# Kernel tuning notes

Measured on AMD Instinct MI355X. Metric: run time of the kernel, lower is better.

## Reference

```python
import jax, jax.numpy as jnp
import numpy as np

E = 131072      # edges per key
MUL = 64        # multiplicity in '64x0e+64x1o'
FEA = MUL * 4   # 64 scalars + 64*3 vector components = 256
RAD = 64        # edge-length embedding width (64x0e)
HID = 128       # MLP hidden (128x0e)
WNUM = 4 * MUL  # 4 uvu paths x 64 per-channel weights = 256


def _mlp(x, W1, b1, g, be, W2):
    # Linear -> LayerNorm -> Gate(silu on scalars) -> last Linear (no bias)
    h = x @ W1 + b1
    mu = h.mean(-1, keepdims=True)
    var = h.var(-1, keepdims=True)
    h = (h - mu) / jnp.sqrt(var + 1e-5) * g + be
    return jax.nn.silu(h) @ W2


def _dtp(fea, vec, w):
    # depthwise (uvu) tensor product of (64x0e+64x1o) x (1x0e+1x1o) -> (64x0e+64x1o)
    x0 = fea[:, :MUL]                       # [E, 64]   0e part
    x1 = fea[:, MUL:].reshape(-1, MUL, 3)   # [E, 64, 3] 1o part
    y0 = vec[:, 0]                          # [E]       0e
    y1 = vec[:, 1:4]                        # [E, 3]    1o
    w1, w2, w3, w4 = jnp.split(w, 4, axis=1)  # each [E, 64]
    inv_s3 = 1.0 / jnp.sqrt(jnp.asarray(3.0, fea.dtype))  # CG(1,1,0) = delta/sqrt(3)
    inv_s2 = 1.0 / jnp.sqrt(jnp.asarray(2.0, fea.dtype))  # per-output path normalization (2 paths each)
    out0 = (w1 * x0 * y0[:, None]
            + w4 * jnp.einsum('eud,ed->eu', x1, y1) * inv_s3) * inv_s2
    out1 = (w2[:, :, None] * x0[:, :, None] * y1[:, None, :]
            + w3[:, :, None] * x1 * y0[:, None, None]) * inv_s2
    return jnp.concatenate([out0, out1.reshape(-1, MUL * 3)], axis=1)


def setup_inputs() -> dict:
    key = jax.random.key(0)
    ks = jax.random.split(key, 16)
    d = {}
    for i, k in enumerate(['a', 'b']):
        d[f'edge_fea_{k}'] = jax.random.normal(ks[i * 3 + 0], (E, FEA), jnp.float32)
        d[f'edge_vec_{k}'] = jax.random.normal(ks[i * 3 + 1], (E, 4), jnp.float32)
        d[f'edge_len_{k}'] = jax.random.uniform(ks[i * 3 + 2], (E, RAD), jnp.float32)
        d[f'W1_{k}'] = jax.random.normal(ks[6 + i * 2], (RAD, HID), jnp.float32) / np.sqrt(RAD)
        d[f'b1_{k}'] = jnp.zeros((HID,), jnp.float32)
        d[f'g_{k}'] = jnp.ones((HID,), jnp.float32)
        d[f'be_{k}'] = jnp.zeros((HID,), jnp.float32)
        d[f'W2_{k}'] = jax.random.normal(ks[10 + i * 2], (HID, WNUM), jnp.float32) / np.sqrt(HID)
    return d


def reference(edge_fea_a, edge_vec_a, edge_len_a, W1_a, b1_a, g_a, be_a, W2_a,
              edge_fea_b, edge_vec_b, edge_len_b, W1_b, b1_b, g_b, be_b, W2_b):
    wa = _mlp(edge_len_a, W1_a, b1_a, g_a, be_a, W2_a)
    wb = _mlp(edge_len_b, W1_b, b1_b, g_b, be_b, W2_b)
    return (_dtp(edge_fea_a, edge_vec_a, wa), _dtp(edge_fea_b, edge_vec_b, wb))
```

## Files before the change

### kernel.cpp

```cpp
#include <hip/hip_runtime.h>

namespace {
constexpr int E_N  = 131072;
constexpr int FEA  = 256;
constexpr int RAD  = 64;
constexpr int HID  = 128;
constexpr int WN   = 256;
constexpr int EPB  = 64;
constexpr int NT   = 256;
constexpr int ASTR = 132;
constexpr int SMEMF = EPB * ASTR;
constexpr int FRAG_HI_SHORTS = 2 * 4 * 16 * 64 * 8;
}

typedef float float2v __attribute__((ext_vector_type(2)));
typedef short short8v __attribute__((ext_vector_type(8)));
typedef float floatx4 __attribute__((ext_vector_type(4)));

__device__ __forceinline__ float2v pkfma_lo(float2v a, float2v b, float2v c) {
    float2v d;
    asm("v_pk_fma_f32 %0, %1, %2, %3 op_sel:[0,0,0] op_sel_hi:[0,1,1]"
        : "=v"(d) : "v"(a), "v"(b), "v"(c));
    return d;
}
__device__ __forceinline__ float2v pkfma_hi(float2v a, float2v b, float2v c) {
    float2v d;
    asm("v_pk_fma_f32 %0, %1, %2, %3 op_sel:[1,0,0] op_sel_hi:[1,1,1]"
        : "=v"(d) : "v"(a), "v"(b), "v"(c));
    return d;
}

__device__ __forceinline__ unsigned bf16rne(float x) {
    const unsigned u = __float_as_uint(x);
    return (u + 0x7FFFu + ((u >> 16) & 1u)) >> 16;
}
__device__ __forceinline__ float bf16tof(unsigned h) {
    return __uint_as_float(h << 16);
}
__device__ __forceinline__ void bf16split(float x, unsigned& hi, unsigned& lo) {
    hi = bf16rne(x);
    lo = bf16rne(x - bf16tof(hi));
}

union FragU { uint4 u; short8v v; };

__global__ __launch_bounds__(64)
void prep_w2(const float* __restrict__ W2a, const float* __restrict__ W2b,
             unsigned short* __restrict__ frag)
{
    const int lane = threadIdx.x;
    const int nb = blockIdx.x, kt = blockIdx.y, pipe = blockIdx.z;
    const float* __restrict__ W2 = pipe ? W2b : W2a;
    const int g = lane >> 4, s = lane & 15;
    unsigned ph[4], pl[4];
    #pragma unroll
    for (int p = 0; p < 4; ++p) {
        const float x0 = W2[(size_t)(32*kt + 8*g + 2*p)     * WN + nb*16 + s];
        const float x1 = W2[(size_t)(32*kt + 8*g + 2*p + 1) * WN + nb*16 + s];
        unsigned h0, l0, h1, l1;
        bf16split(x0, h0, l0);
        bf16split(x1, h1, l1);
        ph[p] = h0 | (h1 << 16);
        pl[p] = l0 | (l1 << 16);
    }
    const size_t fi = (size_t)pipe * 32768 + (size_t)((kt*16 + nb)*64 + lane) * 8;
    *(uint4*)(frag + fi)                  = make_uint4(ph[0], ph[1], ph[2], ph[3]);
    *(uint4*)(frag + FRAG_HI_SHORTS + fi) = make_uint4(pl[0], pl[1], pl[2], pl[3]);
}

__global__ __launch_bounds__(NT, 4)
void fused_mlp_dtp(
    const float* __restrict__ fea_a, const float* __restrict__ vec_a,
    const float* __restrict__ len_a, const float* __restrict__ W1_a,
    const float* __restrict__ b1_a,  const float* __restrict__ g_a,
    const float* __restrict__ be_a,  const float* __restrict__ W2_a,
    const float* __restrict__ fea_b, const float* __restrict__ vec_b,
    const float* __restrict__ len_b, const float* __restrict__ W1_b,
    const float* __restrict__ b1_b,  const float* __restrict__ g_b,
    const float* __restrict__ be_b,  const float* __restrict__ W2_b,
    const unsigned short* __restrict__ fragW,
    float* __restrict__ out)
{
    __shared__ __align__(16) float smem[SMEMF];

    const int pipe = blockIdx.y;
    const float* __restrict__ fea = pipe ? fea_b : fea_a;
    const float* __restrict__ vec = pipe ? vec_b : vec_a;
    const float* __restrict__ len = pipe ? len_b : len_a;
    const float* __restrict__ W1  = pipe ? W1_b  : W1_a;
    const float* __restrict__ b1  = pipe ? b1_b  : b1_a;
    const float* __restrict__ g   = pipe ? g_b   : g_a;
    const float* __restrict__ be  = pipe ? be_b  : be_a;
    float* __restrict__ outp = out + (size_t)pipe * (size_t)E_N * FEA;

    const int t    = threadIdx.x;
    const int lane = t & 63;
    const int wv_  = t >> 6;
    const long e0  = (long)blockIdx.x * EPB;

    {
        const float4* __restrict__ src = (const float4*)(len + e0 * RAD);
        float4* dst = (float4*)smem;
        #pragma unroll
        for (int i = 0; i < (EPB * RAD / 4) / NT; ++i)
            dst[t + i * NT] = src[t + i * NT];
    }
    __syncthreads();

    const int c0 = (t & 31) * 4;
    const int eb = (t >> 5) * 8;
    float2v accA[8], accB[8];
    {
        #pragma unroll
        for (int i = 0; i < 8; ++i) { accA[i] = (float2v)0.f; accB[i] = (float2v)0.f; }

        for (int kg = 0; kg < RAD / 4; ++kg) {
            float4 w0 = *(const float4*)(W1 + (size_t)(kg*4 + 0) * HID + c0);
            float4 w1 = *(const float4*)(W1 + (size_t)(kg*4 + 1) * HID + c0);
            float4 w2 = *(const float4*)(W1 + (size_t)(kg*4 + 2) * HID + c0);
            float4 w3 = *(const float4*)(W1 + (size_t)(kg*4 + 3) * HID + c0);
            const float2v w0A = *(float2v*)&w0, w0B = *((float2v*)&w0 + 1);
            const float2v w1A = *(float2v*)&w1, w1B = *((float2v*)&w1 + 1);
            const float2v w2A = *(float2v*)&w2, w2B = *((float2v*)&w2 + 1);
            const float2v w3A = *(float2v*)&w3, w3B = *((float2v*)&w3 + 1);
            #pragma unroll
            for (int i = 0; i < 8; ++i) {
                float4 lv = *(const float4*)(&smem[(eb + i) * RAD + kg * 4]);
                const float2v lvA = *(float2v*)&lv;
                const float2v lvB = *((float2v*)&lv + 1);
                accA[i] = pkfma_lo(lvA, w0A, accA[i]);
                accB[i] = pkfma_lo(lvA, w0B, accB[i]);
                accA[i] = pkfma_hi(lvA, w1A, accA[i]);
                accB[i] = pkfma_hi(lvA, w1B, accB[i]);
                accA[i] = pkfma_lo(lvB, w2A, accA[i]);
                accB[i] = pkfma_lo(lvB, w2B, accB[i]);
                accA[i] = pkfma_hi(lvB, w3A, accA[i]);
                accB[i] = pkfma_hi(lvB, w3B, accB[i]);
            }
        }
    }
    __syncthreads();

    {
        const float4 bv = *(const float4*)(b1 + c0);
        #pragma unroll
        for (int i = 0; i < 8; ++i) {
            const float4 o = make_float4(accA[i].x + bv.x, accA[i].y + bv.y,
                                         accB[i].x + bv.z, accB[i].y + bv.w);
            *(float4*)(&smem[(eb + i) * ASTR + c0]) = o;
        }
    }
    __syncthreads();

    {
        const int e = t >> 2;
        const int q = t & 3;
        float* __restrict__ row = &smem[e * ASTR + q * 32];
        float hv[32];
        float s = 0.f, s2 = 0.f;
        #pragma unroll
        for (int j = 0; j < 8; ++j) {
            const float4 v = *(const float4*)(row + 4 * j);
            hv[4*j+0] = v.x; hv[4*j+1] = v.y; hv[4*j+2] = v.z; hv[4*j+3] = v.w;
            s  += v.x + v.y + v.z + v.w;
            s2 += v.x*v.x + v.y*v.y + v.z*v.z + v.w*v.w;
        }
        s  += __shfl_xor(s, 1);  s  += __shfl_xor(s, 2);
        s2 += __shfl_xor(s2, 1); s2 += __shfl_xor(s2, 2);
        const float mu  = s * (1.0f / HID);
        float var = s2 * (1.0f / HID) - mu * mu;
        var = fmaxf(var, 0.0f);
        const float inv = rsqrtf(var + 1e-5f);
        const float4* __restrict__ gr  = (const float4*)(g  + q * 32);
        const float4* __restrict__ ber = (const float4*)(be + q * 32);
        #pragma unroll
        for (int j = 0; j < 8; ++j) {
            const float4 gv = gr[j];
            const float4 bv = ber[j];
            const float h0 = (hv[4*j+0] - mu) * inv * gv.x + bv.x;
            const float h1 = (hv[4*j+1] - mu) * inv * gv.y + bv.y;
            const float h2 = (hv[4*j+2] - mu) * inv * gv.z + bv.z;
            const float h3 = (hv[4*j+3] - mu) * inv * gv.w + bv.w;
            float4 o;
            o.x = h0 / (1.0f + __expf(-h0));
            o.y = h1 / (1.0f + __expf(-h1));
            o.z = h2 / (1.0f + __expf(-h2));
            o.w = h3 / (1.0f + __expf(-h3));
            *(float4*)(row + 4 * j) = o;
        }
    }
    __syncthreads();

    const int s_ = lane & 15, g_ = lane >> 4;
    floatx4 acc[16];
    #pragma unroll
    for (int nb = 0; nb < 16; ++nb) {
        acc[nb][0] = 0.f; acc[nb][1] = 0.f; acc[nb][2] = 0.f; acc[nb][3] = 0.f;
    }
    {
        const int eA = wv_ * 16 + s_;
        const unsigned short* __restrict__ fH = fragW + (size_t)pipe * 32768;
        const unsigned short* __restrict__ fL = fH + FRAG_HI_SHORTS;
        for (int kt = 0; kt < 4; ++kt) {
            float xs[8];
            {
                const float4 x0 = *(const float4*)(&smem[eA*ASTR + 32*kt + 8*g_]);
                const float4 x1 = *(const float4*)(&smem[eA*ASTR + 32*kt + 8*g_ + 4]);
                xs[0]=x0.x; xs[1]=x0.y; xs[2]=x0.z; xs[3]=x0.w;
                xs[4]=x1.x; xs[5]=x1.y; xs[6]=x1.z; xs[7]=x1.w;
            }
            FragU ahu, alu;
            {
                unsigned ph[4], pl[4];
                #pragma unroll
                for (int p = 0; p < 4; ++p) {
                    unsigned h0, l0, h1, l1;
                    bf16split(xs[2*p],     h0, l0);
                    bf16split(xs[2*p + 1], h1, l1);
                    ph[p] = h0 | (h1 << 16);
                    pl[p] = l0 | (l1 << 16);
                }
                ahu.u = make_uint4(ph[0], ph[1], ph[2], ph[3]);
                alu.u = make_uint4(pl[0], pl[1], pl[2], pl[3]);
            }
            const short8v ah = ahu.v, al = alu.v;
            const size_t kb = (size_t)(kt * 16) * 512 + (size_t)lane * 8;
            #pragma unroll
            for (int nb = 0; nb < 16; ++nb) {
                const short8v bh = *(const short8v*)(fH + kb + nb * 512);
                const short8v bl = *(const short8v*)(fL + kb + nb * 512);
                acc[nb] = __builtin_amdgcn_mfma_f32_16x16x32_bf16(ah, bh, acc[nb], 0, 0, 0);
                acc[nb] = __builtin_amdgcn_mfma_f32_16x16x32_bf16(ah, bl, acc[nb], 0, 0, 0);
                acc[nb] = __builtin_amdgcn_mfma_f32_16x16x32_bf16(al, bh, acc[nb], 0, 0, 0);
            }
        }
    }
    __syncthreads();

    {
        const float c2 = 0.70710678118654752f;
        const float c3 = 0.40824829046386302f;
        float* sStage = smem + wv_ * 784;
        for (int r = 0; r < 4; ++r) {
            const long e = e0 + wv_ * 16 + 4 * g_ + r;
            const float4 y = *(const float4*)(vec + e * 4);
            const float* __restrict__ fr   = fea  + e * (size_t)FEA;
            float* __restrict__       orow = outp + e * (size_t)FEA;
            #pragma unroll
            for (int q = 0; q < 4; ++q) {
                const int u = 16 * q + s_;
                const float w1 = acc[q     ][r];
                const float w2 = acc[q + 4 ][r];
                const float w3 = acc[q + 8 ][r];
                const float w4 = acc[q + 12][r];
                const float x0  = fr[u];
                const float x1a = fr[64 + 3*u + 0];
                const float x1b = fr[64 + 3*u + 1];
                const float x1c = fr[64 + 3*u + 2];
                const float dot = x1a*y.y + x1b*y.z + x1c*y.w;
                orow[u] = w1*x0*y.x*c2 + w4*dot*c3;
                sStage[g_*196 + 3*u + 0] = (w2*x0*y.y + w3*x1a*y.x) * c2;
                sStage[g_*196 + 3*u + 1] = (w2*x0*y.z + w3*x1b*y.x) * c2;
                sStage[g_*196 + 3*u + 2] = (w2*x0*y.w + w3*x1c*y.x) * c2;
            }
            __syncthreads();
            #pragma unroll
            for (int rr = 0; rr < 3; ++rr) {
                const int flat = rr * 256 + lane * 4;
                const int eloc = flat / 192;
                const int pos  = flat % 192;
                const float4 v = *(const float4*)(&sStage[eloc * 196 + pos]);
                *(float4*)(&outp[(e0 + wv_*16 + 4*eloc + r) * (size_t)FEA + 64 + pos]) = v;
            }
            __syncthreads();
        }
    }
}

extern "C" void kernel_launch(void* const* d_in, const int* in_sizes, int n_in,
                              void* d_out, int out_size, void* d_ws, size_t ws_size,
                              hipStream_t stream) {
    (void)in_sizes; (void)n_in; (void)ws_size; (void)out_size;
    const float* fea_a = (const float*)d_in[0];
    const float* vec_a = (const float*)d_in[1];
    const float* len_a = (const float*)d_in[2];
    const float* W1_a  = (const float*)d_in[3];
    const float* b1_a  = (const float*)d_in[4];
    const float* g_a   = (const float*)d_in[5];
    const float* be_a  = (const float*)d_in[6];
    const float* W2_a  = (const float*)d_in[7];
    const float* fea_b = (const float*)d_in[8];
    const float* vec_b = (const float*)d_in[9];
    const float* len_b = (const float*)d_in[10];
    const float* W1_b  = (const float*)d_in[11];
    const float* b1_b  = (const float*)d_in[12];
    const float* g_b   = (const float*)d_in[13];
    const float* be_b  = (const float*)d_in[14];
    const float* W2_b  = (const float*)d_in[15];
    float* out = (float*)d_out;
    unsigned short* frag = (unsigned short*)d_ws;

    hipLaunchKernelGGL(prep_w2, dim3(16, 4, 2), dim3(64), 0, stream,
                       W2_a, W2_b, frag);

    dim3 grid(E_N / EPB, 2);
    dim3 block(NT);
    hipLaunchKernelGGL(fused_mlp_dtp, grid, block, 0, stream,
                       fea_a, vec_a, len_a, W1_a, b1_a, g_a, be_a, W2_a,
                       fea_b, vec_b, len_b, W1_b, b1_b, g_b, be_b, W2_b,
                       frag, out);
}
```

Baseline: 219.5 us.

## Move first MLP linear to split-bf16 MFMA and fuse LayerNorm into accumulators

```diff
diff --git a/kernel.cpp b/kernel.cpp
--- a/kernel.cpp
+++ b/kernel.cpp
@@ -8,27 +8,16 @@
 constexpr int WN   = 256;
 constexpr int EPB  = 64;
 constexpr int NT   = 256;
+constexpr int LSTR = 68;
 constexpr int ASTR = 132;
 constexpr int SMEMF = EPB * ASTR;
 constexpr int FRAG_HI_SHORTS = 2 * 4 * 16 * 64 * 8;
-}
-
-typedef float float2v __attribute__((ext_vector_type(2)));
+constexpr int W1HI = 2 * FRAG_HI_SHORTS;
+constexpr int W1LO_DELTA = 2 * 2 * 8 * 64 * 8;
+}
+
 typedef short short8v __attribute__((ext_vector_type(8)));
 typedef float floatx4 __attribute__((ext_vector_type(4)));
-
-__device__ __forceinline__ float2v pkfma_lo(float2v a, float2v b, float2v c) {
-    float2v d;
-    asm("v_pk_fma_f32 %0, %1, %2, %3 op_sel:[0,0,0] op_sel_hi:[0,1,1]"
-        : "=v"(d) : "v"(a), "v"(b), "v"(c));
-    return d;
-}
-__device__ __forceinline__ float2v pkfma_hi(float2v a, float2v b, float2v c) {
-    float2v d;
-    asm("v_pk_fma_f32 %0, %1, %2, %3 op_sel:[1,0,0] op_sel_hi:[1,1,1]"
-        : "=v"(d) : "v"(a), "v"(b), "v"(c));
-    return d;
-}
 
 __device__ __forceinline__ unsigned bf16rne(float x) {
     const unsigned u = __float_as_uint(x);
@@ -68,16 +57,39 @@
     *(uint4*)(frag + FRAG_HI_SHORTS + fi) = make_uint4(pl[0], pl[1], pl[2], pl[3]);
 }
 
+__global__ __launch_bounds__(64)
+void prep_w1(const float* __restrict__ W1a, const float* __restrict__ W1b,
+             unsigned short* __restrict__ frag)
+{
+    const int lane = threadIdx.x;
+    const int nb = blockIdx.x, kt = blockIdx.y, pipe = blockIdx.z;
+    const float* __restrict__ W1 = pipe ? W1b : W1a;
+    const int g = lane >> 4, s = lane & 15;
+    unsigned ph[4], pl[4];
+    #pragma unroll
+    for (int p = 0; p < 4; ++p) {
+        const float x0 = W1[(size_t)(32*kt + 8*g + 2*p)     * HID + nb*16 + s];
+        const float x1 = W1[(size_t)(32*kt + 8*g + 2*p + 1) * HID + nb*16 + s];
+        unsigned h0, l0, h1, l1;
+        bf16split(x0, h0, l0);
+        bf16split(x1, h1, l1);
+        ph[p] = h0 | (h1 << 16);
+        pl[p] = l0 | (l1 << 16);
+    }
+    const size_t fi = (size_t)W1HI + (size_t)pipe * 8192
+                    + (size_t)((kt*8 + nb)*64 + lane) * 8;
+    *(uint4*)(frag + fi)              = make_uint4(ph[0], ph[1], ph[2], ph[3]);
+    *(uint4*)(frag + W1LO_DELTA + fi) = make_uint4(pl[0], pl[1], pl[2], pl[3]);
+}
+
 __global__ __launch_bounds__(NT, 4)
 void fused_mlp_dtp(
     const float* __restrict__ fea_a, const float* __restrict__ vec_a,
-    const float* __restrict__ len_a, const float* __restrict__ W1_a,
-    const float* __restrict__ b1_a,  const float* __restrict__ g_a,
-    const float* __restrict__ be_a,  const float* __restrict__ W2_a,
+    const float* __restrict__ len_a, const float* __restrict__ b1_a,
+    const float* __restrict__ g_a,   const float* __restrict__ be_a,
     const float* __restrict__ fea_b, const float* __restrict__ vec_b,
-    const float* __restrict__ len_b, const float* __restrict__ W1_b,
-    const float* __restrict__ b1_b,  const float* __restrict__ g_b,
-    const float* __restrict__ be_b,  const float* __restrict__ W2_b,
+    const float* __restrict__ len_b, const float* __restrict__ b1_b,
+    const float* __restrict__ g_b,   const float* __restrict__ be_b,
     const unsigned short* __restrict__ fragW,
     float* __restrict__ out)
 {
@@ -87,7 +99,6 @@
     const float* __restrict__ fea = pipe ? fea_b : fea_a;
     const float* __restrict__ vec = pipe ? vec_b : vec_a;
     const float* __restrict__ len = pipe ? len_b : len_a;
-    const float* __restrict__ W1  = pipe ? W1_b  : W1_a;
     const float* __restrict__ b1  = pipe ? b1_b  : b1_a;
     const float* __restrict__ g   = pipe ? g_b   : g_a;
     const float* __restrict__ be  = pipe ? be_b  : be_a;
@@ -96,102 +107,110 @@
     const int t    = threadIdx.x;
     const int lane = t & 63;
     const int wv_  = t >> 6;
+    const int s_   = lane & 15, g_ = lane >> 4;
     const long e0  = (long)blockIdx.x * EPB;
 
     {
         const float4* __restrict__ src = (const float4*)(len + e0 * RAD);
-        float4* dst = (float4*)smem;
-        #pragma unroll
-        for (int i = 0; i < (EPB * RAD / 4) / NT; ++i)
-            dst[t + i * NT] = src[t + i * NT];
+        #pragma unroll
+        for (int i = 0; i < (EPB * RAD / 4) / NT; ++i) {
+            const int f = t + i * NT;
+            const float4 v = src[f];
+            const int e = f >> 4, kq = (f & 15) * 4;
+            *(float4*)(&smem[e * LSTR + kq]) = v;
+        }
     }
     __syncthreads();
 
-    const int c0 = (t & 31) * 4;
-    const int eb = (t >> 5) * 8;
-    float2v accA[8], accB[8];
-    {
-        #pragma unroll
-        for (int i = 0; i < 8; ++i) { accA[i] = (float2v)0.f; accB[i] = (float2v)0.f; }
-
-        for (int kg = 0; kg < RAD / 4; ++kg) {
-            float4 w0 = *(const float4*)(W1 + (size_t)(kg*4 + 0) * HID + c0);
-            float4 w1 = *(const float4*)(W1 + (size_t)(kg*4 + 1) * HID + c0);
-            float4 w2 = *(const float4*)(W1 + (size_t)(kg*4 + 2) * HID + c0);
-            float4 w3 = *(const float4*)(W1 + (size_t)(kg*4 + 3) * HID + c0);
-            const float2v w0A = *(float2v*)&w0, w0B = *((float2v*)&w0 + 1);
-            const float2v w1A = *(float2v*)&w1, w1B = *((float2v*)&w1 + 1);
-            const float2v w2A = *(float2v*)&w2, w2B = *((float2v*)&w2 + 1);
-            const float2v w3A = *(float2v*)&w3, w3B = *((float2v*)&w3 + 1);
-            #pragma unroll
-            for (int i = 0; i < 8; ++i) {
-                float4 lv = *(const float4*)(&smem[(eb + i) * RAD + kg * 4]);
-                const float2v lvA = *(float2v*)&lv;
-                const float2v lvB = *((float2v*)&lv + 1);
-                accA[i] = pkfma_lo(lvA, w0A, accA[i]);
-                accB[i] = pkfma_lo(lvA, w0B, accB[i]);
-                accA[i] = pkfma_hi(lvA, w1A, accA[i]);
-                accB[i] = pkfma_hi(lvA, w1B, accB[i]);
-                accA[i] = pkfma_lo(lvB, w2A, accA[i]);
-                accB[i] = pkfma_lo(lvB, w2B, accB[i]);
-                accA[i] = pkfma_hi(lvB, w3A, accA[i]);
-                accB[i] = pkfma_hi(lvB, w3B, accB[i]);
+    floatx4 acc2[8];
+    #pragma unroll
+    for (int nb = 0; nb < 8; ++nb) {
+        acc2[nb][0] = 0.f; acc2[nb][1] = 0.f; acc2[nb][2] = 0.f; acc2[nb][3] = 0.f;
+    }
+    {
+        const int eA = wv_ * 16 + s_;
+        const unsigned short* __restrict__ fH1 = fragW + W1HI + (size_t)pipe * 8192;
+        const unsigned short* __restrict__ fL1 = fH1 + W1LO_DELTA;
+        #pragma unroll
+        for (int kt = 0; kt < 2; ++kt) {
+            float xs[8];
+            {
+                const float4 x0 = *(const float4*)(&smem[eA*LSTR + 32*kt + 8*g_]);
+                const float4 x1 = *(const float4*)(&smem[eA*LSTR + 32*kt + 8*g_ + 4]);
+                xs[0]=x0.x; xs[1]=x0.y; xs[2]=x0.z; xs[3]=x0.w;
+                xs[4]=x1.x; xs[5]=x1.y; xs[6]=x1.z; xs[7]=x1.w;
+            }
+            FragU ahu, alu;
+            {
+                unsigned ph[4], pl[4];
+                #pragma unroll
+                for (int p = 0; p < 4; ++p) {
+                    unsigned h0, l0, h1, l1;
+                    bf16split(xs[2*p],     h0, l0);
+                    bf16split(xs[2*p + 1], h1, l1);
+                    ph[p] = h0 | (h1 << 16);
+                    pl[p] = l0 | (l1 << 16);
+                }
+                ahu.u = make_uint4(ph[0], ph[1], ph[2], ph[3]);
+                alu.u = make_uint4(pl[0], pl[1], pl[2], pl[3]);
+            }
+            const short8v ah = ahu.v, al = alu.v;
+            const size_t kb = (size_t)(kt * 8) * 512 + (size_t)lane * 8;
+            #pragma unroll
+            for (int nb = 0; nb < 8; ++nb) {
+                const short8v bh = *(const short8v*)(fH1 + kb + nb * 512);
+                const short8v bl = *(const short8v*)(fL1 + kb + nb * 512);
+                acc2[nb] = __builtin_amdgcn_mfma_f32_16x16x32_bf16(ah, bh, acc2[nb], 0, 0, 0);
+                acc2[nb] = __builtin_amdgcn_mfma_f32_16x16x32_bf16(ah, bl, acc2[nb], 0, 0, 0);
+                acc2[nb] = __builtin_amdgcn_mfma_f32_16x16x32_bf16(al, bh, acc2[nb], 0, 0, 0);
             }
         }
     }
     __syncthreads();
 
     {
-        const float4 bv = *(const float4*)(b1 + c0);
-        #pragma unroll
-        for (int i = 0; i < 8; ++i) {
-            const float4 o = make_float4(accA[i].x + bv.x, accA[i].y + bv.y,
-                                         accB[i].x + bv.z, accB[i].y + bv.w);
-            *(float4*)(&smem[(eb + i) * ASTR + c0]) = o;
+        float hv[8][4];
+        float sum[4] = {0.f, 0.f, 0.f, 0.f};
+        float sq [4] = {0.f, 0.f, 0.f, 0.f};
+        #pragma unroll
+        for (int nb = 0; nb < 8; ++nb) {
+            const float b1v = b1[16*nb + s_];
+            #pragma unroll
+            for (int r = 0; r < 4; ++r) {
+                const float v = acc2[nb][r] + b1v;
+                hv[nb][r] = v;
+                sum[r] += v;
+                sq [r] += v * v;
+            }
+        }
+        float mu[4], iv[4];
+        #pragma unroll
+        for (int r = 0; r < 4; ++r) {
+            float s1 = sum[r], s2 = sq[r];
+            s1 += __shfl_xor(s1, 1); s1 += __shfl_xor(s1, 2);
+            s1 += __shfl_xor(s1, 4); s1 += __shfl_xor(s1, 8);
+            s2 += __shfl_xor(s2, 1); s2 += __shfl_xor(s2, 2);
+            s2 += __shfl_xor(s2, 4); s2 += __shfl_xor(s2, 8);
+            mu[r] = s1 * (1.0f / HID);
+            float var = s2 * (1.0f / HID) - mu[r] * mu[r];
+            var = fmaxf(var, 0.0f);
+            iv[r] = rsqrtf(var + 1e-5f);
+        }
+        const int rowb = wv_ * 16 + 4 * g_;
+        #pragma unroll
+        for (int nb = 0; nb < 8; ++nb) {
+            const float gv  = g [16*nb + s_];
+            const float bev = be[16*nb + s_];
+            #pragma unroll
+            for (int r = 0; r < 4; ++r) {
+                const float hn = (hv[nb][r] - mu[r]) * iv[r] * gv + bev;
+                const float sl = hn / (1.0f + __expf(-hn));
+                smem[(rowb + r) * ASTR + 16*nb + s_] = sl;
+            }
         }
     }
     __syncthreads();
 
-    {
-        const int e = t >> 2;
-        const int q = t & 3;
-        float* __restrict__ row = &smem[e * ASTR + q * 32];
-        float hv[32];
-        float s = 0.f, s2 = 0.f;
-        #pragma unroll
-        for (int j = 0; j < 8; ++j) {
-            const float4 v = *(const float4*)(row + 4 * j);
-            hv[4*j+0] = v.x; hv[4*j+1] = v.y; hv[4*j+2] = v.z; hv[4*j+3] = v.w;
-            s  += v.x + v.y + v.z + v.w;
-            s2 += v.x*v.x + v.y*v.y + v.z*v.z + v.w*v.w;
-        }
-        s  += __shfl_xor(s, 1);  s  += __shfl_xor(s, 2);
-        s2 += __shfl_xor(s2, 1); s2 += __shfl_xor(s2, 2);
-        const float mu  = s * (1.0f / HID);
-        float var = s2 * (1.0f / HID) - mu * mu;
-        var = fmaxf(var, 0.0f);
-        const float inv = rsqrtf(var + 1e-5f);
-        const float4* __restrict__ gr  = (const float4*)(g  + q * 32);
-        const float4* __restrict__ ber = (const float4*)(be + q * 32);
-        #pragma unroll
-        for (int j = 0; j < 8; ++j) {
-            const float4 gv = gr[j];
-            const float4 bv = ber[j];
-            const float h0 = (hv[4*j+0] - mu) * inv * gv.x + bv.x;
-            const float h1 = (hv[4*j+1] - mu) * inv * gv.y + bv.y;
-            const float h2 = (hv[4*j+2] - mu) * inv * gv.z + bv.z;
-            const float h3 = (hv[4*j+3] - mu) * inv * gv.w + bv.w;
-            float4 o;
-            o.x = h0 / (1.0f + __expf(-h0));
-            o.y = h1 / (1.0f + __expf(-h1));
-            o.z = h2 / (1.0f + __expf(-h2));
-            o.w = h3 / (1.0f + __expf(-h3));
-            *(float4*)(row + 4 * j) = o;
-        }
-    }
-    __syncthreads();
-
-    const int s_ = lane & 15, g_ = lane >> 4;
     floatx4 acc[16];
     #pragma unroll
     for (int nb = 0; nb < 16; ++nb) {
@@ -302,11 +321,13 @@
 
     hipLaunchKernelGGL(prep_w2, dim3(16, 4, 2), dim3(64), 0, stream,
                        W2_a, W2_b, frag);
+    hipLaunchKernelGGL(prep_w1, dim3(8, 2, 2), dim3(64), 0, stream,
+                       W1_a, W1_b, frag);
 
     dim3 grid(E_N / EPB, 2);
     dim3 block(NT);
     hipLaunchKernelGGL(fused_mlp_dtp, grid, block, 0, stream,
-                       fea_a, vec_a, len_a, W1_a, b1_a, g_a, be_a, W2_a,
-                       fea_b, vec_b, len_b, W1_b, b1_b, g_b, be_b, W2_b,
+                       fea_a, vec_a, len_a, b1_a, g_a, be_a,
+                       fea_b, vec_b, len_b, b1_b, g_b, be_b,
                        frag, out);
 }
```

Result: faster. 180.9 us, median of 2 (-17.6%).
